# Kernel optimization log

Hardware: AMD Instinct MI355X
Metric: run time of the kernel (lower is better)

The kernel has to match this reference:

```python
import jax, jax.numpy as jnp
import numpy as np

B, C, H, W = 4, 64, 64, 64
INTER = 16  # in_c // k


def setup_inputs() -> dict:
    key = jax.random.key(0)
    ks = jax.random.split(key, 12)
    sC = 1.0 / np.sqrt(C)
    sI = 1.0 / np.sqrt(INTER)
    return {
        "x":   jax.random.normal(ks[0], (B, C, H, W), dtype=jnp.float32),
        "Wq":  jax.random.normal(ks[1], (INTER, C), dtype=jnp.float32) * sC,
        "bq":  jax.random.normal(ks[2], (INTER,), dtype=jnp.float32) * 0.1,
        "Wk":  jax.random.normal(ks[3], (INTER, C), dtype=jnp.float32) * sC,
        "bk":  jax.random.normal(ks[4], (INTER,), dtype=jnp.float32) * 0.1,
        "wcq": jax.random.normal(ks[5], (INTER,), dtype=jnp.float32) * sI,
        "wck": jax.random.normal(ks[6], (INTER,), dtype=jnp.float32) * sI,
        "Wv":  jax.random.normal(ks[7], (C, C), dtype=jnp.float32) * sC,
        "bv":  jax.random.normal(ks[8], (C,), dtype=jnp.float32) * 0.1,
        "Wg":  jax.random.normal(ks[9], (C, C), dtype=jnp.float32) * sC,
        "bg":  jax.random.normal(ks[10], (C,), dtype=jnp.float32) * 0.1,
    }


def reference(x, Wq, bq, Wk, bk, wcq, wck, Wv, bv, Wg, bg):
    b_, c_, h_, w_ = x.shape
    n = h_ * w_
    xf = x.reshape(b_, c_, n)  # (B, C, N)
    # 1x1 conv projections (per-pixel linear maps)
    q = jnp.einsum('oc,bcn->bon', Wq, xf) + bq[None, :, None]  # (B, inter, N)
    k = jnp.einsum('oc,bcn->bon', Wk, xf) + bk[None, :, None]  # (B, inter, N)
    # concat_conv (1x1, no bias) over [q_i ; k_j] decomposes into an outer sum:
    # energy[b,i,j] = wcq . q[b,:,i] + wck . k[b,:,j]
    a = jnp.einsum('o,bon->bn', wcq, q)  # (B, N)
    d = jnp.einsum('o,bon->bn', wck, k)  # (B, N)
    energy = jax.nn.elu(a[:, :, None] + d[:, None, :])  # (B, N, N)
    energy = energy / (1.5 * jnp.sum(energy, axis=1, keepdims=True))
    v = jnp.einsum('oc,bcn->bon', Wv, xf) + bv[None, :, None]  # (B, C, N)
    out = jnp.einsum('bci,bij->bcj', v, energy)  # (B, C, N)
    # gamma 1x1 conv
    out = jnp.einsum('oc,bcn->bon', Wg, out) + bg[None, :, None]
    return out.reshape(b_, c_, h_, w_)
```

## Files before the change

kernel.cpp:

```cpp
#include <hip/hip_runtime.h>
#include <math.h>

#define NB 4096

#define LEAFo  0
#define MASTo  768
#define RELo   864
#define GHo    1120
#define MEMSET_BYTES 70016
#define VGo    17504
#define ASo    1066080
#define PERMo  1082464
#define Po     1098848
#define PSEAo  1148000
#define PSAo   1148256

__device__ __forceinline__ void gst(float* p, float v) {
    __hip_atomic_store(p, v, __ATOMIC_RELAXED, __HIP_MEMORY_SCOPE_AGENT);
}
__device__ __forceinline__ void gsti(int* p, int v) {
    __hip_atomic_store(p, v, __ATOMIC_RELAXED, __HIP_MEMORY_SCOPE_AGENT);
}

__device__ __forceinline__ int bucket_of(float v) {
    int k = (int)((v + 16.0f) * 128.0f);
    k = k < 0 ? 0 : k;
    k = k > (NB - 1) ? (NB - 1) : k;
    return k;
}

__device__ __forceinline__ void gbar(int* wsi, int idx) {
    __syncthreads();
    if (threadIdx.x == 0) {
        int leaf = blockIdx.x & 7;
        bool bcast = false;
        int old = __hip_atomic_fetch_add(wsi + LEAFo + (idx * 8 + leaf) * 32, 1,
                                         __ATOMIC_RELAXED, __HIP_MEMORY_SCOPE_AGENT);
        if (old == 31) {
            int m = __hip_atomic_fetch_add(wsi + MASTo + idx * 32, 1,
                                           __ATOMIC_RELAXED, __HIP_MEMORY_SCOPE_AGENT);
            if (m == 7) {
#pragma unroll
                for (int i = 0; i < 8; i++)
                    __hip_atomic_store(wsi + RELo + i * 32, idx + 1,
                                       __ATOMIC_RELAXED, __HIP_MEMORY_SCOPE_AGENT);
                bcast = true;
            }
        }
        if (!bcast) {
            const int* myrel = wsi + RELo + leaf * 32;
            while (__hip_atomic_load(myrel, __ATOMIC_RELAXED, __HIP_MEMORY_SCOPE_AGENT) <= idx)
                __builtin_amdgcn_s_sleep(1);
        }
    }
    __syncthreads();
}

__global__ __launch_bounds__(1024, 1) void k_fused(
        const float* __restrict__ x,
        const float* __restrict__ Wq, const float* __restrict__ bq,
        const float* __restrict__ Wk, const float* __restrict__ bk,
        const float* __restrict__ wcq, const float* __restrict__ wck,
        const float* __restrict__ Wv, const float* __restrict__ bv,
        const float* __restrict__ Wg, const float* __restrict__ bg,
        float* __restrict__ ws, float* __restrict__ out) {
    __shared__ float smem[13824];
    int tid = threadIdx.x;
    int bid = blockIdx.x;
    int b = bid >> 6, t6 = bid & 63;
    int* wsi = (int*)ws;

    float myA = 0.f, myD = 0.f;
    int   myQ = 0;

    {
        float* xt  = smem;
        float* wt  = smem + 4608;
        float* wgT = smem + 9216;
        float* wqe = smem + 13376, *wke = smem + 13440, *bvg = smem + 13504, *misc = smem + 13568;
        const float4* xb4 = (const float4*)(x + (size_t)b * 64 * 4096);
        float4 xr;
        {
            int c = tid >> 4, nl4 = tid & 15;
            xr = xb4[c * 1024 + t6 * 16 + nl4];
        }
        {
            const float4* wg4 = (const float4*)Wg;
            int o = tid >> 4, q4 = tid & 15;
            float4 g = wg4[tid];
            int m0 = q4 * 4;
            wgT[(m0 + 0) * 65 + o] = g.x; wgT[(m0 + 1) * 65 + o] = g.y;
            wgT[(m0 + 2) * 65 + o] = g.z; wgT[(m0 + 3) * 65 + o] = g.w;
        }
        if (tid < 64) {
            float s1 = 0.f, s2 = 0.f;
            for (int o = 0; o < 16; o++) { s1 += wcq[o] * Wq[o * 64 + tid]; s2 += wck[o] * Wk[o * 64 + tid]; }
            wqe[tid] = s1; wke[tid] = s2;
        } else if (tid == 64) {
            float s = 0.f; for (int o = 0; o < 16; o++) s += wcq[o] * bq[o]; misc[0] = s;
        } else if (tid == 65) {
            float s = 0.f; for (int o = 0; o < 16; o++) s += wck[o] * bk[o]; misc[1] = s;
        }
        {
            int c = tid >> 4, nl4 = tid & 15;
            *(float4*)&xt[c * 72 + nl4 * 4] = xr;
        }
        __syncthreads();
        {
            int o = tid & 63, c0 = (tid >> 6) * 4;
            float acc[4];
#pragma unroll
            for (int k = 0; k < 4; k++) acc[k] = 0.f;
            for (int m = 0; m < 64; m++) {
                float wg = wgT[m * 65 + o];
                float4 a0 = *(const float4*)(Wv + m * 64 + c0);
                acc[0] += wg * a0.x; acc[1] += wg * a0.y; acc[2] += wg * a0.z; acc[3] += wg * a0.w;
            }
#pragma unroll
            for (int k = 0; k < 4; k++) wt[(c0 + k) * 72 + o] = acc[k];
        }
        if (tid < 64) {
            float s3 = 0.f;
            for (int m = 0; m < 64; m++) s3 += wgT[m * 65 + tid] * bv[m];
            bvg[tid] = s3;
        }
        __syncthreads();
        if (tid < 64) {
            float s1 = misc[0], s2 = misc[1];
            for (int c = 0; c < 64; c++) {
                float xv = xt[c * 72 + tid];
                s1 += wqe[c] * xv; s2 += wke[c] * xv;
            }
            myA = s1; myD = s2;
            atomicAdd(&wsi[GHo + b * 4096 + bucket_of(s1)], 1);
        }
        {
            int o = tid & 63, nl0 = (tid >> 6) * 4;
            float acc[4];
            float bo = bvg[o];
#pragma unroll
            for (int k = 0; k < 4; k++) acc[k] = bo;
            for (int c = 0; c < 64; c++) {
                float wv = wt[c * 72 + o];
                const float* xr2 = &xt[c * 72 + nl0];
#pragma unroll
                for (int k = 0; k < 4; k++) acc[k] += wv * xr2[k];
            }
#pragma unroll
            for (int k = 0; k < 4; k++)
                gst(&ws[VGo + ((size_t)(b * 4096) + t6 * 64 + nl0 + k) * 64 + o], acc[k]);
        }
    }
    gbar(wsi, 0);

    {
        unsigned int* hist = (unsigned int*)smem;
        unsigned int* wtot = hist + 4096;
        int* gh_b = wsi + GHo + b * 4096;
#pragma unroll 4
        for (int i = tid; i < NB; i += 1024) hist[i] = (unsigned int)gh_b[i] & 0xFFFFu;
        __syncthreads();
        int lane = tid & 63, w = tid >> 6;
        unsigned int s = 0u; int base = tid * 4;
#pragma unroll
        for (int k = 0; k < 4; k++) s += hist[base + k];
        unsigned int inc = s;
        for (int off = 1; off < 64; off <<= 1) {
            unsigned int u = __shfl_up(inc, off);
            if (lane >= off) inc += u;
        }
        if (lane == 63) wtot[w] = inc;
        __syncthreads();
        unsigned int run = inc - s;
        for (int w2 = 0; w2 < w; w2++) run += wtot[w2];
        for (int k = 0; k < 4; k++) {
            unsigned int h = hist[base + k];
            hist[base + k] = run;
            run += h;
        }
        __syncthreads();
        if (tid < 64) {
            myQ = ((int)hist[bucket_of(-myD)] + 32) >> 6;
            int i = t6 * 64 + tid;
            int kb = bucket_of(myA);
            int old = atomicAdd(&gh_b[kb], 0x10000);
            int r = (int)hist[kb] + (old >> 16);
            gst(&ws[ASo + b * 4096 + r], myA);
            gsti((int*)ws + PERMo + b * 4096 + r, i);
        }
    }
    gbar(wsi, 1);

    {
        int c = tid & 63, w = tid >> 6;
        int r0 = t6 * 64 + w * 4;
        const int* perm = (const int*)ws + PERMo;
        int pk[4]; float avs[4], wvs[4];
#pragma unroll
        for (int k = 0; k < 4; k++) pk[k] = perm[b * 4096 + r0 + k];
#pragma unroll
        for (int k = 0; k < 4; k++) avs[k] = ws[ASo + b * 4096 + r0 + k];
#pragma unroll
        for (int k = 0; k < 4; k++) wvs[k] = ws[VGo + ((size_t)(b * 4096) + pk[k]) * 64 + c];
        float s1 = 0.f, s2 = 0.f, s3 = 0.f, sea_w = 0.f, sa_w = 0.f;
#pragma unroll
        for (int k = 0; k < 4; k++) {
            float ea = expf(avs[k]);
            s1 += wvs[k]; s2 += wvs[k] * ea; s3 += wvs[k] * avs[k];
            sea_w += ea; sa_w += avs[k];
        }
        float* partL = smem;
        float* wsc   = smem + 3072;
        partL[(w * 3 + 0) * 64 + c] = s1;
        partL[(w * 3 + 1) * 64 + c] = s2;
        partL[(w * 3 + 2) * 64 + c] = s3;
        if (c == 0) { wsc[w] = sea_w; wsc[16 + w] = sa_w; }
        __syncthreads();
        if (tid < 192) {
            int g = tid >> 6, cc = tid & 63;
            float sum = 0.f;
#pragma unroll
            for (int ww = 0; ww < 16; ww++) sum += partL[(ww * 3 + g) * 64 + cc];
            gst(&ws[Po + (b * 64 + t6) * 192 + tid], sum);
        } else if (tid == 192) {
            float sum = 0.f;
#pragma unroll
            for (int ww = 0; ww < 16; ww++) sum += wsc[ww];
            gst(&ws[PSEAo + b * 64 + t6], sum);
        } else if (tid == 193) {
            float sum = 0.f;
#pragma unroll
            for (int ww = 0; ww < 16; ww++) sum += wsc[16 + ww];
            gst(&ws[PSAo + b * 64 + t6], sum);
        }
    }
    gbar(wsi, 2);

    {
        float* CP     = smem;
        float* cpsea  = smem + 12545;
        float* cpsa   = smem + 12610;
        float* djs    = smem + 12675;
        float* edjs   = smem + 12739;
        float* invden = smem + 12803;
        int*   qarr   = (int*)(smem + 12867);
        float* bgs    = smem + 12931;
        if (tid < 192) {
            float v[64];
#pragma unroll
            for (int ch = 0; ch < 64; ch++) v[ch] = ws[Po + b * 12288 + ch * 192 + tid];
            float r = 0.f;
#pragma unroll
            for (int q = 0; q < 64; q++) { CP[q * 193 + tid] = r; r += v[q]; }
            CP[64 * 193 + tid] = r;
        } else if (tid == 192) {
            float v[64];
#pragma unroll
            for (int ch = 0; ch < 64; ch++) v[ch] = ws[PSEAo + b * 64 + ch];
            float r = 0.f;
#pragma unroll
            for (int q = 0; q < 64; q++) { cpsea[q] = r; r += v[q]; }
            cpsea[64] = r;
        } else if (tid == 193) {
            float v[64];
#pragma unroll
            for (int ch = 0; ch < 64; ch++) v[ch] = ws[PSAo + b * 64 + ch];
            float r = 0.f;
#pragma unroll
            for (int q = 0; q < 64; q++) { cpsa[q] = r; r += v[q]; }
            cpsa[64] = r;
        }
        if (tid < 64) bgs[tid] = bg[tid];
        __syncthreads();
        int j0 = t6 * 64;
        if (tid < 64) {
            float dj = myD;
            float edj = expf(dj);
            int q = myQ;
            float den = 1.5f * ((cpsa[64] - cpsa[q]) + dj * (float)(4096 - 64 * q)
                                - (float)(64 * q) + edj * cpsea[q]);
            qarr[tid] = q; djs[tid] = dj; edjs[tid] = edj; invden[tid] = 1.0f / den;
        }
        __syncthreads();
        {
            int jl = tid & 63, cq = tid >> 6;
            float dj = djs[jl], edj = edjs[jl], inv = invden[jl];
            int qb = qarr[jl] * 193;
#pragma unroll
            for (int cc = cq; cc < 64; cc += 16) {
                float c1 = CP[qb + cc], c2 = CP[qb + 64 + cc], c3 = CP[qb + 128 + cc];
                float t1 = CP[64 * 193 + cc], t3 = CP[64 * 193 + 128 + cc];
                float num = (t3 - c3) + dj * t1 - (1.0f + dj) * c1 + edj * c2;
                out[((size_t)(b * 64 + cc)) * 4096 + j0 + jl] = num * inv + bgs[cc];
            }
        }
    }
}

extern "C" void kernel_launch(void* const* d_in, const int* in_sizes, int n_in,
                              void* d_out, int out_size, void* d_ws, size_t ws_size,
                              hipStream_t stream) {
    const float* x   = (const float*)d_in[0];
    const float* Wq  = (const float*)d_in[1];
    const float* bq  = (const float*)d_in[2];
    const float* Wk  = (const float*)d_in[3];
    const float* bk  = (const float*)d_in[4];
    const float* wcq = (const float*)d_in[5];
    const float* wck = (const float*)d_in[6];
    const float* Wv  = (const float*)d_in[7];
    const float* bv  = (const float*)d_in[8];
    const float* Wg  = (const float*)d_in[9];
    const float* bg  = (const float*)d_in[10];
    float* ws  = (float*)d_ws;
    float* out = (float*)d_out;

    hipMemsetAsync(d_ws, 0, MEMSET_BYTES, stream);
    k_fused<<<256, 1024, 0, stream>>>(x, Wq, bq, Wk, bk, wcq, wck, Wv, bv, Wg, bg, ws, out);
}
```

Before: 103.2 us.

## Keep value projection in registers and scatter into per-block LDS chunk tables

Instead of writing the projected values to global memory and then gathering them through a sorted permutation, each block keeps its values in registers and atomically accumulates per-chunk partial sums (v, v*exp(a), v*a, plus exp(a) and a totals) into a shared-memory table. It then writes that table to the workspace, and a reduction stage sums the 64 per-block tables for each batch. The grid barriers are also made per-batch instead of global. This removes the permutation and sorted-value global writes and the scattered gather. It adds LDS atomics, a much larger workspace table (64 blocks x 12416 floats per batch) and a reduction pass over it.

```diff
diff --git a/kernel.cpp b/kernel.cpp
--- a/kernel.cpp
+++ b/kernel.cpp
@@ -4,21 +4,14 @@
 #define NB 4096
 
 #define LEAFo  0
-#define MASTo  768
-#define RELo   864
-#define GHo    1120
-#define MEMSET_BYTES 70016
-#define VGo    17504
-#define ASo    1066080
-#define PERMo  1082464
-#define Po     1098848
-#define PSEAo  1148000
-#define PSAo   1148256
+#define MASTo  3072
+#define RELo   3456
+#define GHo    4480
+#define MEMSET_BYTES 83456
+#define TBLo   20864
+#define Ro     3199360
 
 __device__ __forceinline__ void gst(float* p, float v) {
-    __hip_atomic_store(p, v, __ATOMIC_RELAXED, __HIP_MEMORY_SCOPE_AGENT);
-}
-__device__ __forceinline__ void gsti(int* p, int v) {
     __hip_atomic_store(p, v, __ATOMIC_RELAXED, __HIP_MEMORY_SCOPE_AGENT);
 }
 
@@ -29,26 +22,26 @@
     return k;
 }
 
-__device__ __forceinline__ void gbar(int* wsi, int idx) {
+__device__ __forceinline__ void gbar(int* wsi, int idx, int b, int t6) {
     __syncthreads();
     if (threadIdx.x == 0) {
-        int leaf = blockIdx.x & 7;
+        int leaf = t6 & 7;
         bool bcast = false;
-        int old = __hip_atomic_fetch_add(wsi + LEAFo + (idx * 8 + leaf) * 32, 1,
+        int old = __hip_atomic_fetch_add(wsi + LEAFo + ((idx * 4 + b) * 8 + leaf) * 32, 1,
                                          __ATOMIC_RELAXED, __HIP_MEMORY_SCOPE_AGENT);
-        if (old == 31) {
-            int m = __hip_atomic_fetch_add(wsi + MASTo + idx * 32, 1,
+        if (old == 7) {
+            int m = __hip_atomic_fetch_add(wsi + MASTo + (idx * 4 + b) * 32, 1,
                                            __ATOMIC_RELAXED, __HIP_MEMORY_SCOPE_AGENT);
             if (m == 7) {
 #pragma unroll
                 for (int i = 0; i < 8; i++)
-                    __hip_atomic_store(wsi + RELo + i * 32, idx + 1,
+                    __hip_atomic_store(wsi + RELo + (b * 8 + i) * 32, idx + 1,
                                        __ATOMIC_RELAXED, __HIP_MEMORY_SCOPE_AGENT);
                 bcast = true;
             }
         }
         if (!bcast) {
-            const int* myrel = wsi + RELo + leaf * 32;
+            const int* myrel = wsi + RELo + (b * 8 + (t6 & 7)) * 32;
             while (__hip_atomic_load(myrel, __ATOMIC_RELAXED, __HIP_MEMORY_SCOPE_AGENT) <= idx)
                 __builtin_amdgcn_s_sleep(1);
         }
@@ -72,6 +65,7 @@
 
     float myA = 0.f, myD = 0.f;
     int   myQ = 0;
+    float vg[4];
 
     {
         float* xt  = smem;
@@ -136,26 +130,25 @@
         }
         {
             int o = tid & 63, nl0 = (tid >> 6) * 4;
-            float acc[4];
             float bo = bvg[o];
 #pragma unroll
-            for (int k = 0; k < 4; k++) acc[k] = bo;
+            for (int k = 0; k < 4; k++) vg[k] = bo;
             for (int c = 0; c < 64; c++) {
                 float wv = wt[c * 72 + o];
                 const float* xr2 = &xt[c * 72 + nl0];
 #pragma unroll
-                for (int k = 0; k < 4; k++) acc[k] += wv * xr2[k];
-            }
-#pragma unroll
-            for (int k = 0; k < 4; k++)
-                gst(&ws[VGo + ((size_t)(b * 4096) + t6 * 64 + nl0 + k) * 64 + o], acc[k]);
-        }
-    }
-    gbar(wsi, 0);
+                for (int k = 0; k < 4; k++) vg[k] += wv * xr2[k];
+            }
+        }
+    }
+    gbar(wsi, 0, b, t6);
 
     {
         unsigned int* hist = (unsigned int*)smem;
         unsigned int* wtot = hist + 4096;
+        int*   chkL  = (int*)(smem + 13440);
+        float* expaL = smem + 13504;
+        float* avalL = smem + 13568;
         int* gh_b = wsi + GHo + b * 4096;
 #pragma unroll 4
         for (int i = tid; i < NB; i += 1024) hist[i] = (unsigned int)gh_b[i] & 0xFFFFu;
@@ -181,94 +174,78 @@
         __syncthreads();
         if (tid < 64) {
             myQ = ((int)hist[bucket_of(-myD)] + 32) >> 6;
-            int i = t6 * 64 + tid;
             int kb = bucket_of(myA);
             int old = atomicAdd(&gh_b[kb], 0x10000);
             int r = (int)hist[kb] + (old >> 16);
-            gst(&ws[ASo + b * 4096 + r], myA);
-            gsti((int*)ws + PERMo + b * 4096 + r, i);
-        }
-    }
-    gbar(wsi, 1);
-
-    {
-        int c = tid & 63, w = tid >> 6;
-        int r0 = t6 * 64 + w * 4;
-        const int* perm = (const int*)ws + PERMo;
-        int pk[4]; float avs[4], wvs[4];
-#pragma unroll
-        for (int k = 0; k < 4; k++) pk[k] = perm[b * 4096 + r0 + k];
-#pragma unroll
-        for (int k = 0; k < 4; k++) avs[k] = ws[ASo + b * 4096 + r0 + k];
-#pragma unroll
-        for (int k = 0; k < 4; k++) wvs[k] = ws[VGo + ((size_t)(b * 4096) + pk[k]) * 64 + c];
-        float s1 = 0.f, s2 = 0.f, s3 = 0.f, sea_w = 0.f, sa_w = 0.f;
+            chkL[tid]  = r >> 6;
+            expaL[tid] = expf(myA);
+            avalL[tid] = myA;
+        }
+        __syncthreads();
+    }
+
+    {
+        float* tbl   = smem;
+        int*   chkL  = (int*)(smem + 13440);
+        float* expaL = smem + 13504;
+        float* avalL = smem + 13568;
+        for (int i = tid; i < 12416; i += 1024) tbl[i] = 0.f;
+        __syncthreads();
+        int o = tid & 63, nl0 = (tid >> 6) * 4;
 #pragma unroll
         for (int k = 0; k < 4; k++) {
-            float ea = expf(avs[k]);
-            s1 += wvs[k]; s2 += wvs[k] * ea; s3 += wvs[k] * avs[k];
-            sea_w += ea; sa_w += avs[k];
-        }
-        float* partL = smem;
-        float* wsc   = smem + 3072;
-        partL[(w * 3 + 0) * 64 + c] = s1;
-        partL[(w * 3 + 1) * 64 + c] = s2;
-        partL[(w * 3 + 2) * 64 + c] = s3;
-        if (c == 0) { wsc[w] = sea_w; wsc[16 + w] = sa_w; }
-        __syncthreads();
-        if (tid < 192) {
-            int g = tid >> 6, cc = tid & 63;
-            float sum = 0.f;
-#pragma unroll
-            for (int ww = 0; ww < 16; ww++) sum += partL[(ww * 3 + g) * 64 + cc];
-            gst(&ws[Po + (b * 64 + t6) * 192 + tid], sum);
-        } else if (tid == 192) {
-            float sum = 0.f;
-#pragma unroll
-            for (int ww = 0; ww < 16; ww++) sum += wsc[ww];
-            gst(&ws[PSEAo + b * 64 + t6], sum);
-        } else if (tid == 193) {
-            float sum = 0.f;
-#pragma unroll
-            for (int ww = 0; ww < 16; ww++) sum += wsc[16 + ww];
-            gst(&ws[PSAo + b * 64 + t6], sum);
-        }
-    }
-    gbar(wsi, 2);
+            int p = nl0 + k;
+            int ch = chkL[p];
+            float v = vg[k];
+            atomicAdd(&tbl[ch * 194 + o],       v);
+            atomicAdd(&tbl[ch * 194 + 64 + o],  v * expaL[p]);
+            atomicAdd(&tbl[ch * 194 + 128 + o], v * avalL[p]);
+        }
+        if (tid < 64) {
+            int ch = chkL[tid];
+            atomicAdd(&tbl[ch * 194 + 192], expaL[tid]);
+            atomicAdd(&tbl[ch * 194 + 193], avalL[tid]);
+        }
+        __syncthreads();
+        float* dst = ws + TBLo + (size_t)bid * 12416;
+        for (int i = tid; i < 12416; i += 1024) gst(&dst[i], tbl[i]);
+    }
+    gbar(wsi, 1, b, t6);
+
+    {
+        float* part = smem;
+        int g = tid / 194;
+        int col = tid - g * 194;
+        if (g < 4) {
+            const float* src = ws + TBLo + (size_t)(b * 64) * 12416 + t6 * 194 + col;
+            float s = 0.f;
+#pragma unroll
+            for (int t = 0; t < 16; t++) s += src[(size_t)(g * 16 + t) * 12416];
+            part[g * 208 + col] = s;
+        }
+        __syncthreads();
+        if (tid < 194) {
+            float s = part[tid] + part[208 + tid] + part[416 + tid] + part[624 + tid];
+            gst(&ws[Ro + (size_t)(b * 64 + t6) * 194 + tid], s);
+        }
+    }
+    gbar(wsi, 2, b, t6);
 
     {
         float* CP     = smem;
-        float* cpsea  = smem + 12545;
-        float* cpsa   = smem + 12610;
         float* djs    = smem + 12675;
         float* edjs   = smem + 12739;
         float* invden = smem + 12803;
         int*   qarr   = (int*)(smem + 12867);
         float* bgs    = smem + 12931;
-        if (tid < 192) {
+        if (tid < 194) {
             float v[64];
 #pragma unroll
-            for (int ch = 0; ch < 64; ch++) v[ch] = ws[Po + b * 12288 + ch * 192 + tid];
+            for (int ch = 0; ch < 64; ch++) v[ch] = ws[Ro + (size_t)(b * 64 + ch) * 194 + tid];
             float r = 0.f;
 #pragma unroll
-            for (int q = 0; q < 64; q++) { CP[q * 193 + tid] = r; r += v[q]; }
-            CP[64 * 193 + tid] = r;
-        } else if (tid == 192) {
-            float v[64];
-#pragma unroll
-            for (int ch = 0; ch < 64; ch++) v[ch] = ws[PSEAo + b * 64 + ch];
-            float r = 0.f;
-#pragma unroll
-            for (int q = 0; q < 64; q++) { cpsea[q] = r; r += v[q]; }
-            cpsea[64] = r;
-        } else if (tid == 193) {
-            float v[64];
-#pragma unroll
-            for (int ch = 0; ch < 64; ch++) v[ch] = ws[PSAo + b * 64 + ch];
-            float r = 0.f;
-#pragma unroll
-            for (int q = 0; q < 64; q++) { cpsa[q] = r; r += v[q]; }
-            cpsa[64] = r;
+            for (int q = 0; q < 64; q++) { CP[q * 195 + tid] = r; r += v[q]; }
+            CP[64 * 195 + tid] = r;
         }
         if (tid < 64) bgs[tid] = bg[tid];
         __syncthreads();
@@ -277,19 +254,20 @@
             float dj = myD;
             float edj = expf(dj);
             int q = myQ;
-            float den = 1.5f * ((cpsa[64] - cpsa[q]) + dj * (float)(4096 - 64 * q)
-                                - (float)(64 * q) + edj * cpsea[q]);
+            float den = 1.5f * ((CP[64 * 195 + 193] - CP[q * 195 + 193])
+                                + dj * (float)(4096 - 64 * q)
+                                - (float)(64 * q) + edj * CP[q * 195 + 192]);
             qarr[tid] = q; djs[tid] = dj; edjs[tid] = edj; invden[tid] = 1.0f / den;
         }
         __syncthreads();
         {
             int jl = tid & 63, cq = tid >> 6;
             float dj = djs[jl], edj = edjs[jl], inv = invden[jl];
-            int qb = qarr[jl] * 193;
+            int qb = qarr[jl] * 195;
 #pragma unroll
             for (int cc = cq; cc < 64; cc += 16) {
                 float c1 = CP[qb + cc], c2 = CP[qb + 64 + cc], c3 = CP[qb + 128 + cc];
-                float t1 = CP[64 * 193 + cc], t3 = CP[64 * 193 + 128 + cc];
+                float t1 = CP[64 * 195 + cc], t3 = CP[64 * 195 + 128 + cc];
                 float num = (t3 - c3) + dj * t1 - (1.0f + dj) * c1 + edj * c2;
                 out[((size_t)(b * 64 + cc)) * 4096 + j0 + jl] = num * inv + bgs[cc];
             }
```

Result: slower. 217.4 us (+110.6%).

## Hoist weight folding into prep kernel and use per-batch grid barriers

Applied to the files above, without the earlier changes.

Moves the per-block Wg·Wv folding, bias folding and q/k weight collapsing into a single-block prep kernel that also zeroes the workspace, replacing the memset. The fused kernel now just loads the precomputed folded weights. Its grid barriers become per-batch, each covering the 64 blocks of one batch instead of all 256, so batches no longer wait on each other. The cost is an extra serial kernel launch running on one block, plus a redesigned barrier tree that must stay correct.

```diff
diff --git a/kernel.cpp b/kernel.cpp
--- a/kernel.cpp
+++ b/kernel.cpp
@@ -4,16 +4,21 @@
 #define NB 4096
 
 #define LEAFo  0
-#define MASTo  768
-#define RELo   864
-#define GHo    1120
-#define MEMSET_BYTES 70016
-#define VGo    17504
-#define ASo    1066080
-#define PERMo  1082464
-#define Po     1098848
-#define PSEAo  1148000
-#define PSAo   1148256
+#define MASTo  3072
+#define RELo   3456
+#define GHo    4480
+#define ZERO_F4 5216
+#define WTo    20864
+#define BVGo   24960
+#define WQEo   25024
+#define WKEo   25088
+#define MISCo  25152
+#define VGo    25216
+#define ASo    1073792
+#define PERMo  1090176
+#define Po     1106560
+#define PSEAo  1155712
+#define PSAo   1155968
 
 __device__ __forceinline__ void gst(float* p, float v) {
     __hip_atomic_store(p, v, __ATOMIC_RELAXED, __HIP_MEMORY_SCOPE_AGENT);
@@ -29,26 +34,26 @@
     return k;
 }
 
-__device__ __forceinline__ void gbar(int* wsi, int idx) {
+__device__ __forceinline__ void gbar(int* wsi, int idx, int b, int t6) {
     __syncthreads();
     if (threadIdx.x == 0) {
-        int leaf = blockIdx.x & 7;
+        int leaf = t6 & 7;
         bool bcast = false;
-        int old = __hip_atomic_fetch_add(wsi + LEAFo + (idx * 8 + leaf) * 32, 1,
+        int old = __hip_atomic_fetch_add(wsi + LEAFo + ((idx * 4 + b) * 8 + leaf) * 32, 1,
                                          __ATOMIC_RELAXED, __HIP_MEMORY_SCOPE_AGENT);
-        if (old == 31) {
-            int m = __hip_atomic_fetch_add(wsi + MASTo + idx * 32, 1,
+        if (old == 7) {
+            int m = __hip_atomic_fetch_add(wsi + MASTo + (idx * 4 + b) * 32, 1,
                                            __ATOMIC_RELAXED, __HIP_MEMORY_SCOPE_AGENT);
             if (m == 7) {
 #pragma unroll
                 for (int i = 0; i < 8; i++)
-                    __hip_atomic_store(wsi + RELo + i * 32, idx + 1,
+                    __hip_atomic_store(wsi + RELo + (b * 8 + i) * 32, idx + 1,
                                        __ATOMIC_RELAXED, __HIP_MEMORY_SCOPE_AGENT);
                 bcast = true;
             }
         }
         if (!bcast) {
-            const int* myrel = wsi + RELo + leaf * 32;
+            const int* myrel = wsi + RELo + (b * 8 + leaf) * 32;
             while (__hip_atomic_load(myrel, __ATOMIC_RELAXED, __HIP_MEMORY_SCOPE_AGENT) <= idx)
                 __builtin_amdgcn_s_sleep(1);
         }
@@ -56,13 +61,43 @@
     __syncthreads();
 }
 
-__global__ __launch_bounds__(1024, 1) void k_fused(
-        const float* __restrict__ x,
+__global__ __launch_bounds__(1024) void k_prep(
         const float* __restrict__ Wq, const float* __restrict__ bq,
         const float* __restrict__ Wk, const float* __restrict__ bk,
         const float* __restrict__ wcq, const float* __restrict__ wck,
         const float* __restrict__ Wv, const float* __restrict__ bv,
-        const float* __restrict__ Wg, const float* __restrict__ bg,
+        const float* __restrict__ Wg, float* __restrict__ ws) {
+    int tid = threadIdx.x;
+    float4 z = make_float4(0.f, 0.f, 0.f, 0.f);
+    for (int i = tid; i < ZERO_F4; i += 1024) ((float4*)ws)[i] = z;
+    if (tid < 64) {
+        float s1 = 0.f, s2 = 0.f, s3 = 0.f;
+        for (int o = 0; o < 16; o++) { s1 += wcq[o] * Wq[o * 64 + tid]; s2 += wck[o] * Wk[o * 64 + tid]; }
+        for (int m = 0; m < 64; m++) s3 += Wg[tid * 64 + m] * bv[m];
+        ws[WQEo + tid] = s1; ws[WKEo + tid] = s2; ws[BVGo + tid] = s3;
+    } else if (tid == 64) {
+        float s = 0.f; for (int o = 0; o < 16; o++) s += wcq[o] * bq[o]; ws[MISCo] = s;
+    } else if (tid == 65) {
+        float s = 0.f; for (int o = 0; o < 16; o++) s += wck[o] * bk[o]; ws[MISCo + 1] = s;
+    }
+    {
+        int o = tid & 63, c0 = (tid >> 6) * 4;
+        float acc[4];
+#pragma unroll
+        for (int k = 0; k < 4; k++) acc[k] = 0.f;
+        for (int m = 0; m < 64; m++) {
+            float wg = Wg[o * 64 + m];
+            float4 a0 = *(const float4*)(Wv + m * 64 + c0);
+            acc[0] += wg * a0.x; acc[1] += wg * a0.y; acc[2] += wg * a0.z; acc[3] += wg * a0.w;
+        }
+#pragma unroll
+        for (int k = 0; k < 4; k++) ws[WTo + (c0 + k) * 64 + o] = acc[k];
+    }
+}
+
+__global__ __launch_bounds__(1024, 1) void k_fused(
+        const float* __restrict__ x,
+        const float* __restrict__ bg,
         float* __restrict__ ws, float* __restrict__ out) {
     __shared__ float smem[13824];
     int tid = threadIdx.x;
@@ -76,57 +111,21 @@
     {
         float* xt  = smem;
         float* wt  = smem + 4608;
-        float* wgT = smem + 9216;
-        float* wqe = smem + 13376, *wke = smem + 13440, *bvg = smem + 13504, *misc = smem + 13568;
+        float* wqe = smem + 9216, *wke = smem + 9280;
         const float4* xb4 = (const float4*)(x + (size_t)b * 64 * 4096);
-        float4 xr;
         {
             int c = tid >> 4, nl4 = tid & 15;
-            xr = xb4[c * 1024 + t6 * 16 + nl4];
+            float4 xr = xb4[c * 1024 + t6 * 16 + nl4];
+            *(float4*)&xt[c * 72 + nl4 * 4] = xr;
         }
         {
-            const float4* wg4 = (const float4*)Wg;
-            int o = tid >> 4, q4 = tid & 15;
-            float4 g = wg4[tid];
-            int m0 = q4 * 4;
-            wgT[(m0 + 0) * 65 + o] = g.x; wgT[(m0 + 1) * 65 + o] = g.y;
-            wgT[(m0 + 2) * 65 + o] = g.z; wgT[(m0 + 3) * 65 + o] = g.w;
-        }
+            int c = tid >> 4, o0 = (tid & 15) * 4;
+            *(float4*)&wt[c * 72 + o0] = *(const float4*)&ws[WTo + c * 64 + o0];
+        }
+        if (tid < 64) { wqe[tid] = ws[WQEo + tid]; wke[tid] = ws[WKEo + tid]; }
+        __syncthreads();
         if (tid < 64) {
-            float s1 = 0.f, s2 = 0.f;
-            for (int o = 0; o < 16; o++) { s1 += wcq[o] * Wq[o * 64 + tid]; s2 += wck[o] * Wk[o * 64 + tid]; }
-            wqe[tid] = s1; wke[tid] = s2;
-        } else if (tid == 64) {
-            float s = 0.f; for (int o = 0; o < 16; o++) s += wcq[o] * bq[o]; misc[0] = s;
-        } else if (tid == 65) {
-            float s = 0.f; for (int o = 0; o < 16; o++) s += wck[o] * bk[o]; misc[1] = s;
-        }
-        {
-            int c = tid >> 4, nl4 = tid & 15;
-            *(float4*)&xt[c * 72 + nl4 * 4] = xr;
-        }
-        __syncthreads();
-        {
-            int o = tid & 63, c0 = (tid >> 6) * 4;
-            float acc[4];
-#pragma unroll
-            for (int k = 0; k < 4; k++) acc[k] = 0.f;
-            for (int m = 0; m < 64; m++) {
-                float wg = wgT[m * 65 + o];
-                float4 a0 = *(const float4*)(Wv + m * 64 + c0);
-                acc[0] += wg * a0.x; acc[1] += wg * a0.y; acc[2] += wg * a0.z; acc[3] += wg * a0.w;
-            }
-#pragma unroll
-            for (int k = 0; k < 4; k++) wt[(c0 + k) * 72 + o] = acc[k];
-        }
-        if (tid < 64) {
-            float s3 = 0.f;
-            for (int m = 0; m < 64; m++) s3 += wgT[m * 65 + tid] * bv[m];
-            bvg[tid] = s3;
-        }
-        __syncthreads();
-        if (tid < 64) {
-            float s1 = misc[0], s2 = misc[1];
+            float s1 = ws[MISCo], s2 = ws[MISCo + 1];
             for (int c = 0; c < 64; c++) {
                 float xv = xt[c * 72 + tid];
                 s1 += wqe[c] * xv; s2 += wke[c] * xv;
@@ -137,7 +136,7 @@
         {
             int o = tid & 63, nl0 = (tid >> 6) * 4;
             float acc[4];
-            float bo = bvg[o];
+            float bo = ws[BVGo + o];
 #pragma unroll
             for (int k = 0; k < 4; k++) acc[k] = bo;
             for (int c = 0; c < 64; c++) {
@@ -151,7 +150,7 @@
                 gst(&ws[VGo + ((size_t)(b * 4096) + t6 * 64 + nl0 + k) * 64 + o], acc[k]);
         }
     }
-    gbar(wsi, 0);
+    gbar(wsi, 0, b, t6);
 
     {
         unsigned int* hist = (unsigned int*)smem;
@@ -189,7 +188,7 @@
             gsti((int*)ws + PERMo + b * 4096 + r, i);
         }
     }
-    gbar(wsi, 1);
+    gbar(wsi, 1, b, t6);
 
     {
         int c = tid & 63, w = tid >> 6;
@@ -234,7 +233,7 @@
             gst(&ws[PSAo + b * 64 + t6], sum);
         }
     }
-    gbar(wsi, 2);
+    gbar(wsi, 2, b, t6);
 
     {
         float* CP     = smem;
@@ -314,6 +313,6 @@
     float* ws  = (float*)d_ws;
     float* out = (float*)d_out;
 
-    hipMemsetAsync(d_ws, 0, MEMSET_BYTES, stream);
-    k_fused<<<256, 1024, 0, stream>>>(x, Wq, bq, Wk, bk, wcq, wck, Wv, bv, Wg, bg, ws, out);
-}
+    k_prep<<<1, 1024, 0, stream>>>(Wq, bq, Wk, bk, wcq, wck, Wv, bv, Wg, ws);
+    k_fused<<<256, 1024, 0, stream>>>(x, bg, ws, out);
+}
```

After: 109.6 us. 6.2% more time.

## Use per-batch grid barriers and scatter Wv-projected values directly in sorted order

Applied to the files above, without the earlier changes.

The grid-wide barrier becomes a per-batch barrier. Each batch's 64 blocks synchronize through their own leaf, master and release counters, so different batches no longer wait on each other. The projected values are kept in registers until after ranking and then written straight to their sorted positions. This removes the permutation array and the indirect gather in the next phase. The cost is a scattered write pattern for the value rows and a larger zero-initialized workspace for the extra barrier counters.

```diff
diff --git a/kernel.cpp b/kernel.cpp
--- a/kernel.cpp
+++ b/kernel.cpp
@@ -4,21 +4,17 @@
 #define NB 4096
 
 #define LEAFo  0
-#define MASTo  768
-#define RELo   864
-#define GHo    1120
-#define MEMSET_BYTES 70016
-#define VGo    17504
-#define ASo    1066080
-#define PERMo  1082464
-#define Po     1098848
-#define PSEAo  1148000
-#define PSAo   1148256
+#define MASTo  3072
+#define RELo   3456
+#define GHo    4480
+#define MEMSET_BYTES 83456
+#define VGSo   20864
+#define ASo    1069440
+#define Po     1085824
+#define PSEAo  1134976
+#define PSAo   1135232
 
 __device__ __forceinline__ void gst(float* p, float v) {
-    __hip_atomic_store(p, v, __ATOMIC_RELAXED, __HIP_MEMORY_SCOPE_AGENT);
-}
-__device__ __forceinline__ void gsti(int* p, int v) {
     __hip_atomic_store(p, v, __ATOMIC_RELAXED, __HIP_MEMORY_SCOPE_AGENT);
 }
 
@@ -29,26 +25,26 @@
     return k;
 }
 
-__device__ __forceinline__ void gbar(int* wsi, int idx) {
+__device__ __forceinline__ void gbar(int* wsi, int idx, int b, int t6) {
     __syncthreads();
     if (threadIdx.x == 0) {
-        int leaf = blockIdx.x & 7;
+        int leaf = t6 & 7;
         bool bcast = false;
-        int old = __hip_atomic_fetch_add(wsi + LEAFo + (idx * 8 + leaf) * 32, 1,
+        int old = __hip_atomic_fetch_add(wsi + LEAFo + ((idx * 4 + b) * 8 + leaf) * 32, 1,
                                          __ATOMIC_RELAXED, __HIP_MEMORY_SCOPE_AGENT);
-        if (old == 31) {
-            int m = __hip_atomic_fetch_add(wsi + MASTo + idx * 32, 1,
+        if (old == 7) {
+            int m = __hip_atomic_fetch_add(wsi + MASTo + (idx * 4 + b) * 32, 1,
                                            __ATOMIC_RELAXED, __HIP_MEMORY_SCOPE_AGENT);
             if (m == 7) {
 #pragma unroll
                 for (int i = 0; i < 8; i++)
-                    __hip_atomic_store(wsi + RELo + i * 32, idx + 1,
+                    __hip_atomic_store(wsi + RELo + (b * 8 + i) * 32, idx + 1,
                                        __ATOMIC_RELAXED, __HIP_MEMORY_SCOPE_AGENT);
                 bcast = true;
             }
         }
         if (!bcast) {
-            const int* myrel = wsi + RELo + leaf * 32;
+            const int* myrel = wsi + RELo + (b * 8 + leaf) * 32;
             while (__hip_atomic_load(myrel, __ATOMIC_RELAXED, __HIP_MEMORY_SCOPE_AGENT) <= idx)
                 __builtin_amdgcn_s_sleep(1);
         }
@@ -72,6 +68,7 @@
 
     float myA = 0.f, myD = 0.f;
     int   myQ = 0;
+    float vg[4];
 
     {
         float* xt  = smem;
@@ -136,26 +133,23 @@
         }
         {
             int o = tid & 63, nl0 = (tid >> 6) * 4;
-            float acc[4];
             float bo = bvg[o];
 #pragma unroll
-            for (int k = 0; k < 4; k++) acc[k] = bo;
+            for (int k = 0; k < 4; k++) vg[k] = bo;
             for (int c = 0; c < 64; c++) {
                 float wv = wt[c * 72 + o];
                 const float* xr2 = &xt[c * 72 + nl0];
 #pragma unroll
-                for (int k = 0; k < 4; k++) acc[k] += wv * xr2[k];
-            }
-#pragma unroll
-            for (int k = 0; k < 4; k++)
-                gst(&ws[VGo + ((size_t)(b * 4096) + t6 * 64 + nl0 + k) * 64 + o], acc[k]);
-        }
-    }
-    gbar(wsi, 0);
+                for (int k = 0; k < 4; k++) vg[k] += wv * xr2[k];
+            }
+        }
+    }
+    gbar(wsi, 0, b, t6);
 
     {
         unsigned int* hist = (unsigned int*)smem;
         unsigned int* wtot = hist + 4096;
+        int* rnk = (int*)(smem + 13632);
         int* gh_b = wsi + GHo + b * 4096;
 #pragma unroll 4
         for (int i = tid; i < NB; i += 1024) hist[i] = (unsigned int)gh_b[i] & 0xFFFFu;
@@ -181,27 +175,32 @@
         __syncthreads();
         if (tid < 64) {
             myQ = ((int)hist[bucket_of(-myD)] + 32) >> 6;
-            int i = t6 * 64 + tid;
             int kb = bucket_of(myA);
             int old = atomicAdd(&gh_b[kb], 0x10000);
             int r = (int)hist[kb] + (old >> 16);
             gst(&ws[ASo + b * 4096 + r], myA);
-            gsti((int*)ws + PERMo + b * 4096 + r, i);
-        }
-    }
-    gbar(wsi, 1);
+            rnk[tid] = r;
+        }
+        __syncthreads();
+        {
+            int o = tid & 63, g = tid >> 6;
+#pragma unroll
+            for (int k = 0; k < 4; k++) {
+                int r = rnk[g * 4 + k];
+                gst(&ws[VGSo + ((size_t)(b * 4096) + r) * 64 + o], vg[k]);
+            }
+        }
+    }
+    gbar(wsi, 1, b, t6);
 
     {
         int c = tid & 63, w = tid >> 6;
         int r0 = t6 * 64 + w * 4;
-        const int* perm = (const int*)ws + PERMo;
-        int pk[4]; float avs[4], wvs[4];
-#pragma unroll
-        for (int k = 0; k < 4; k++) pk[k] = perm[b * 4096 + r0 + k];
+        float avs[4], wvs[4];
 #pragma unroll
         for (int k = 0; k < 4; k++) avs[k] = ws[ASo + b * 4096 + r0 + k];
 #pragma unroll
-        for (int k = 0; k < 4; k++) wvs[k] = ws[VGo + ((size_t)(b * 4096) + pk[k]) * 64 + c];
+        for (int k = 0; k < 4; k++) wvs[k] = ws[VGSo + ((size_t)(b * 4096) + r0 + k) * 64 + c];
         float s1 = 0.f, s2 = 0.f, s3 = 0.f, sea_w = 0.f, sa_w = 0.f;
 #pragma unroll
         for (int k = 0; k < 4; k++) {
@@ -234,7 +233,7 @@
             gst(&ws[PSAo + b * 64 + t6], sum);
         }
     }
-    gbar(wsi, 2);
+    gbar(wsi, 2, b, t6);
 
     {
         float* CP     = smem;
```

Result: slower. 193.5 us (+87.4%).
